# Kernel optimization log

Measured on AMD Instinct MI355X. Metric: run time of the kernel, lower is better.

The kernel has to match this reference:

```python
import jax, jax.numpy as jnp
import numpy as np

MASK_FILL = jnp.float32(-2**32 + 1)

def dice(x, alpha):
    # x: (S, B, F); batch-dim (dim=0) mean/std, unbiased std like torch.std
    avg = x.mean(axis=0)
    std = jnp.std(x, axis=0, ddof=1)
    p = jax.nn.sigmoid((x - avg) / std)
    return x * p + alpha * x * (1.0 - p)

def setup_inputs() -> dict:
    key = jax.random.key(0)
    ks = jax.random.split(key, 12)
    S, B, D = 200, 1024, 128          # seq_len, batch, 2H
    F = 4 * D                          # num_features = 512
    L1, L2 = 80, 40
    inp = {
        "query": jax.random.normal(ks[0], (B, D), jnp.float32),
        "facts": jax.random.normal(ks[1], (S, B, D), jnp.float32),
        "mask": jax.random.randint(ks[2], (S, B), 0, 2).astype(bool),
        "W1": jax.random.normal(ks[3], (F, L1), jnp.float32) / np.sqrt(F),
        "b1": jnp.zeros((L1,), jnp.float32),
        "a1": jnp.zeros((1,), jnp.float32),
        "W2": jax.random.normal(ks[4], (L1, L2), jnp.float32) / np.sqrt(L1),
        "b2": jnp.zeros((L2,), jnp.float32),
        "a2": jnp.zeros((1,), jnp.float32),
        "W3": jax.random.normal(ks[5], (L2, 1), jnp.float32) / np.sqrt(L2),
        "b3": jnp.zeros((1,), jnp.float32),
    }
    return inp

def reference(query, facts, mask, W1, b1, a1, W2, b2, a2, W3, b3):
    S, B, D = facts.shape
    # faithful to torch: tile along feature dim then reshape (permutes elements)
    q2 = jnp.tile(query, (1, S)).reshape(S, B, D)
    x = jnp.concatenate([q2, facts, q2 * facts, q2 - facts], axis=-1)  # (S,B,4D)
    h = dice(jnp.einsum('sbf,fl->sbl', x, W1) + b1, a1)
    h = dice(jnp.einsum('sbf,fl->sbl', h, W2) + b2, a2)
    logits = (jnp.einsum('sbf,fl->sbl', h, W3) + b3).squeeze(-1)  # (S,B)
    masked = jnp.where(mask, logits, MASK_FILL)
    normalized = jax.nn.softmax(masked, axis=0)
    return normalized[..., None] * facts  # (S,B,D)
```

## Files before the change

### kernel.cpp

```cpp
#include <hip/hip_runtime.h>
#include <hip/hip_bf16.h>
#include <math.h>

#define SS 200
#define BB 1024
#define DD 128
#define FF 512
#define LL1 80
#define LL2 40
#define PP (SS*BB)
#define MASK_FILL_F (-4294967295.0f)
#define NTILE 13

typedef short bf16x8 __attribute__((ext_vector_type(8)));
typedef float f32x4  __attribute__((ext_vector_type(4)));

static __device__ __forceinline__ unsigned short f2bf(float x) {
    __hip_bfloat16 h = __float2bfloat16(x);
    return *reinterpret_cast<unsigned short*>(&h);
}
static __device__ __forceinline__ float bf2f(unsigned short u) {
    __hip_bfloat16 h = *reinterpret_cast<__hip_bfloat16*>(&u);
    return __bfloat162float(h);
}
static __device__ __forceinline__ void split8(const float* x, bf16x8& ah, bf16x8& al) {
#pragma unroll
    for (int j = 0; j < 8; ++j) {
        unsigned u = __float_as_uint(x[j]);
        ah[j] = (short)(u >> 16);
        float hi = __uint_as_float(u & 0xffff0000u);
        al[j] = (short)f2bf(x[j] - hi);
    }
}
static __device__ __forceinline__ float fast_sigmoid(float t) {
    return __builtin_amdgcn_rcpf(1.f + __expf(-t));
}

__global__ void k_prep_all(const float* __restrict__ W1, const float* __restrict__ W2,
                           const unsigned char* __restrict__ mask,
                           unsigned short* __restrict__ bfr1,
                           unsigned short* __restrict__ bfr2, int* __restrict__ flag) {
    const int blk = blockIdx.x;
    if (blk == 35) {
        if (threadIdx.x < 64) {
            const uchar4 u = ((const uchar4*)mask)[threadIdx.x];
            const bool f = ((u.y | u.z) | u.w) != 0;
            const unsigned long long anyf = __ballot(f);
            if (threadIdx.x == 0) *flag = (anyf != 0ull) ? 1 : 0;
        }
        return;
    }
    if (blk < 30) {
        int t = blk * 256 + threadIdx.x;
        if (t >= 120 * 64) return;
        int lane = t & 63;
        int fid  = t >> 6;
        int nt   = fid % 5;
        int hl   = (fid / 5) % 2;
        int step = (fid / 10) % 6;
        int h    = fid / 60;
        int ktL  = step / 3;
        int seg  = step - 3 * ktL;
        int kt   = h * 2 + ktL;
        int n     = nt * 16 + (lane & 15);
        int kbase = kt * 32 + (lane >> 4) * 8;
        unsigned short* o = bfr1 + (size_t)t * 8;
#pragma unroll
        for (int j = 0; j < 8; ++j) {
            int k = kbase + j;
            float w;
            if (seg == 0)      w = W1[k * LL1 + n] + W1[(384 + k) * LL1 + n];
            else if (seg == 1) w = W1[(128 + k) * LL1 + n] - W1[(384 + k) * LL1 + n];
            else               w = W1[(256 + k) * LL1 + n];
            unsigned short hb = f2bf(w);
            o[j] = (hl == 0) ? hb : f2bf(w - bf2f(hb));
        }
    } else {
        int t = (blk - 30) * 256 + threadIdx.x;
        if (t >= 18 * 64) return;
        int lane = t & 63;
        int fid  = t >> 6;
        int hl   = fid & 1;
        int nt   = (fid >> 1) % 3;
        int kt   = fid / 6;
        int n  = nt * 16 + (lane & 15);
        int kb = kt * 32 + (lane >> 4) * 8;
        unsigned short* o = bfr2 + (size_t)t * 8;
#pragma unroll
        for (int j = 0; j < 8; ++j) {
            int k = kb + j;
            float w = (k < LL1 && n < LL2) ? W2[k * LL2 + n] : 0.f;
            unsigned short hb = f2bf(w);
            o[j] = (hl == 0) ? hb : f2bf(w - bf2f(hb));
        }
    }
}

__global__ __launch_bounds__(256, 2) void k1_mfma(
    const float* __restrict__ query, const float* __restrict__ facts,
    const unsigned short* __restrict__ bfr, const float* __restrict__ b1,
    float* __restrict__ z1) {
    const int tid  = threadIdx.x;
    const int lane = tid & 63;
    const int m    = lane & 15;
    const int quad = lane >> 4;
    const int pw   = blockIdx.x * 128 + (tid >> 6) * 32;

    __shared__ __align__(16) unsigned short lbuf[15360];

    f32x4 acc[2][5];
#pragma unroll
    for (int t = 0; t < 2; ++t)
#pragma unroll
        for (int nt = 0; nt < 5; ++nt) acc[t][nt] = (f32x4){0.f, 0.f, 0.f, 0.f};

    int pr[2], qr[2];
#pragma unroll
    for (int t = 0; t < 2; ++t) {
        pr[t] = pw + t * 16 + m;
        qr[t] = pr[t] / SS;
    }

#pragma unroll 1
    for (int kt = 0; kt < 4; ++kt) {
        const int dbase = kt * 32 + quad * 8;
        float q8[2][8], f8[2][8];
#pragma unroll
        for (int t = 0; t < 2; ++t) {
            const float* qp = query + (size_t)qr[t] * DD + dbase;
            const float* fp = facts + (size_t)pr[t] * DD + dbase;
            *(float4*)&q8[t][0] = *(const float4*)qp;
            *(float4*)&q8[t][4] = *(const float4*)(qp + 4);
            *(float4*)&f8[t][0] = *(const float4*)fp;
            *(float4*)&f8[t][4] = *(const float4*)(fp + 4);
        }
        if (kt) __syncthreads();
        {
            const int4* src = (const int4*)bfr + kt * 1920;
#pragma unroll
            for (int it = 0; it < 8; ++it) {
                int idx = it * 256 + tid;
                if (idx < 1920) ((int4*)lbuf)[idx] = src[idx];
            }
        }
        __syncthreads();

#pragma unroll
        for (int seg = 0; seg < 3; ++seg) {
            bf16x8 Bh[5], Bl[5];
#pragma unroll
            for (int nt = 0; nt < 5; ++nt) {
                Bh[nt] = *(const bf16x8*)&lbuf[((seg * 2 + 0) * 5 + nt) * 512 + lane * 8];
                Bl[nt] = *(const bf16x8*)&lbuf[((seg * 2 + 1) * 5 + nt) * 512 + lane * 8];
            }
#pragma unroll
            for (int t = 0; t < 2; ++t) {
                float x8[8];
#pragma unroll
                for (int j = 0; j < 8; ++j)
                    x8[j] = (seg == 0) ? q8[t][j]
                          : (seg == 1 ? f8[t][j] : q8[t][j] * f8[t][j]);
                bf16x8 ah, al;
                split8(x8, ah, al);
#pragma unroll
                for (int nt = 0; nt < 5; ++nt) {
                    acc[t][nt] = __builtin_amdgcn_mfma_f32_16x16x32_bf16(ah, Bh[nt], acc[t][nt], 0, 0, 0);
                    acc[t][nt] = __builtin_amdgcn_mfma_f32_16x16x32_bf16(al, Bh[nt], acc[t][nt], 0, 0, 0);
                    acc[t][nt] = __builtin_amdgcn_mfma_f32_16x16x32_bf16(ah, Bl[nt], acc[t][nt], 0, 0, 0);
                }
            }
        }
    }
#pragma unroll
    for (int t = 0; t < 2; ++t)
#pragma unroll
        for (int nt = 0; nt < 5; ++nt) {
            const int n = nt * 16 + m;
            const float bias = b1[n];
#pragma unroll
            for (int r = 0; r < 4; ++r)
                z1[(size_t)(pw + t * 16 + quad * 4 + r) * LL1 + n] = acc[t][nt][r] + bias;
        }
}

__global__ __launch_bounds__(512) void k_light(
    const float* __restrict__ z1, const unsigned short* __restrict__ bfr2,
    const float* __restrict__ a1, const float* __restrict__ b2,
    const float* __restrict__ a2, const float* __restrict__ W3,
    const float* __restrict__ b3, const void* __restrict__ mask,
    const int* __restrict__ flag, float* __restrict__ wbufT) {
    const int tid  = threadIdx.x;
    const int w    = tid >> 6;
    const int lane = tid & 63;
    const int m    = lane & 15;
    const int quad = lane >> 4;
    const int b    = blockIdx.x;

    __shared__ __align__(16) float z1f[NTILE * 16 * 81 + 16];
    __shared__ float psum[480], pssq[480];
    __shared__ float smean[LL1], sistd[LL1];
    __shared__ float sw3[LL2];
    __shared__ float red[8];

    {
        for (int i = tid; i < SS * 20; i += 512) {
            const int s = i / 20;
            const int o = i - s * 20;
            float4 v = ((const float4*)z1)[(size_t)(s * BB + b) * 20 + o];
            float* d = &z1f[s * 81 + o * 4];
            d[0] = v.x; d[1] = v.y; d[2] = v.z; d[3] = v.w;
        }
        for (int i = tid; i < 8 * 81 + 16; i += 512) z1f[SS * 81 + i] = 0.f;
    }
    __syncthreads();

    if (tid < 480) {
        const int l = tid % LL1, c = tid / LL1;
        const int s0 = c * 34;
        const int s1 = (s0 + 34 < SS) ? s0 + 34 : SS;
        float sum = 0.f, ssq = 0.f;
        for (int s = s0; s < s1; ++s) {
            float v = z1f[s * 81 + l];
            sum += v;
            ssq = fmaf(v, v, ssq);
        }
        psum[c * LL1 + l] = sum;
        pssq[c * LL1 + l] = ssq;
    }
    __syncthreads();
    if (tid < LL1) {
        float sum = 0.f, ssq = 0.f;
#pragma unroll
        for (int c = 0; c < 6; ++c) {
            sum += psum[c * LL1 + tid];
            ssq += pssq[c * LL1 + tid];
        }
        float mn  = sum * (1.f / SS);
        float var = (ssq - (float)SS * mn * mn) * (1.f / (SS - 1));
        smean[tid] = mn;
        sistd[tid] = rsqrtf(var);
    }
    __syncthreads();

    const float alpha1 = *a1;
    f32x4 acc2[2][3];
#pragma unroll
    for (int t = 0; t < 2; ++t)
#pragma unroll
        for (int nt = 0; nt < 3; ++nt) acc2[t][nt] = (f32x4){0.f, 0.f, 0.f, 0.f};

    int tile[2];
    bool tl[2];
#pragma unroll
    for (int t = 0; t < 2; ++t) {
        tile[t] = t * 8 + w;
        tl[t]   = (tile[t] < NTILE);
    }

#pragma unroll
    for (int kt = 0; kt < 3; ++kt) {
        bf16x8 Bh[3], Bl[3];
#pragma unroll
        for (int nt = 0; nt < 3; ++nt) {
            Bh[nt] = *(const bf16x8*)(bfr2 + (size_t)((kt * 3 + nt) * 2 + 0) * 512 + lane * 8);
            Bl[nt] = *(const bf16x8*)(bfr2 + (size_t)((kt * 3 + nt) * 2 + 1) * 512 + lane * 8);
        }
        const int kb = kt * 32 + quad * 8;
        const bool lv = (kt < 2 || quad < 2);
#pragma unroll
        for (int t = 0; t < 2; ++t) {
            if (!tl[t]) continue;
            float x8[8];
            if (lv) {
                const float* zr = &z1f[(tile[t] * 16 + m) * 81 + kb];
#pragma unroll
                for (int j = 0; j < 8; ++j) {
                    float v  = zr[j];
                    float pp = fast_sigmoid((v - smean[kb + j]) * sistd[kb + j]);
                    x8[j] = v * (alpha1 + (1.f - alpha1) * pp);
                }
            } else {
#pragma unroll
                for (int j = 0; j < 8; ++j) x8[j] = 0.f;
            }
            bf16x8 ah, al;
            split8(x8, ah, al);
#pragma unroll
            for (int nt = 0; nt < 3; ++nt) {
                acc2[t][nt] = __builtin_amdgcn_mfma_f32_16x16x32_bf16(ah, Bh[nt], acc2[t][nt], 0, 0, 0);
                acc2[t][nt] = __builtin_amdgcn_mfma_f32_16x16x32_bf16(al, Bh[nt], acc2[t][nt], 0, 0, 0);
                acc2[t][nt] = __builtin_amdgcn_mfma_f32_16x16x32_bf16(ah, Bl[nt], acc2[t][nt], 0, 0, 0);
            }
        }
    }
    __syncthreads();

    {
        float b2v[3];
#pragma unroll
        for (int nt = 0; nt < 3; ++nt) {
            const int n = nt * 16 + m;
            b2v[nt] = (n < LL2) ? b2[n] : 0.f;
        }
#pragma unroll
        for (int t = 0; t < 2; ++t) {
            if (!tl[t]) continue;
#pragma unroll
            for (int r = 0; r < 4; ++r) {
                const int srow = tile[t] * 16 + quad * 4 + r;
                if (srow >= SS) continue;
#pragma unroll
                for (int nt = 0; nt < 3; ++nt) {
                    const int n = nt * 16 + m;
                    if (n < LL2) z1f[srow * 41 + n] = acc2[t][nt][r] + b2v[nt];
                }
            }
        }
    }
    __syncthreads();

    if (tid < 480) {
        const int l = tid % LL2, c = tid / LL2;
        const int s0 = c * 17;
        const int s1 = (s0 + 17 < SS) ? s0 + 17 : SS;
        float sum = 0.f, ssq = 0.f;
        for (int s = s0; s < s1; ++s) {
            float v = z1f[s * 41 + l];
            sum += v;
            ssq = fmaf(v, v, ssq);
        }
        psum[c * LL2 + l] = sum;
        pssq[c * LL2 + l] = ssq;
    }
    __syncthreads();
    if (tid < LL2) {
        float sum = 0.f, ssq = 0.f;
#pragma unroll
        for (int c = 0; c < 12; ++c) {
            sum += psum[c * LL2 + tid];
            ssq += pssq[c * LL2 + tid];
        }
        float mn  = sum * (1.f / SS);
        float var = (ssq - (float)SS * mn * mn) * (1.f / (SS - 1));
        smean[tid] = mn;
        sistd[tid] = rsqrtf(var);
        sw3[tid]   = W3[tid];
    }
    __syncthreads();

    const float alpha2 = *a2;
    const int boolLayout = *flag;
    float logit = -3.0e38f;
    if (tid < SS) {
        float dot = b3[0];
#pragma unroll
        for (int k = 0; k < LL2; ++k) {
            float v  = z1f[tid * 41 + k];
            float pp = fast_sigmoid((v - smean[k]) * sistd[k]);
            float hh = v * (pp + alpha2 * (1.f - pp));
            dot = fmaf(hh, sw3[k], dot);
        }
        const int mi = tid * BB + b;
        const bool mk = boolLayout ? (((const unsigned char*)mask)[mi] != 0)
                                   : (((const int*)mask)[mi] != 0);
        logit = mk ? dot : MASK_FILL_F;
    }
    float v = logit;
#pragma unroll
    for (int off = 1; off < 64; off <<= 1) v = fmaxf(v, __shfl_xor(v, off, 64));
    if (lane == 0) red[w] = v;
    __syncthreads();
    float smax = red[0];
#pragma unroll
    for (int i = 1; i < 8; ++i) smax = fmaxf(smax, red[i]);
    __syncthreads();
    const float e = (tid < SS) ? __expf(logit - smax) : 0.f;
    v = e;
#pragma unroll
    for (int off = 1; off < 64; off <<= 1) v += __shfl_xor(v, off, 64);
    if (lane == 0) red[w] = v;
    __syncthreads();
    float ssum = red[0];
#pragma unroll
    for (int i = 1; i < 8; ++i) ssum += red[i];
    const float inv = __builtin_amdgcn_rcpf(ssum);
    if (tid < SS) wbufT[(size_t)b * SS + tid] = e * inv;
}

__global__ __launch_bounds__(256) void k4_scale(
    const float* __restrict__ wbufT, const float* __restrict__ facts,
    float* __restrict__ out) {
    int i = blockIdx.x * 256 + threadIdx.x;
    int p = i >> 5;
    float w = wbufT[(size_t)(p & (BB - 1)) * SS + (p >> 10)];
    float4 f = ((const float4*)facts)[i];
    float4 o;
    o.x = f.x * w; o.y = f.y * w; o.z = f.z * w; o.w = f.w * w;
    ((float4*)out)[i] = o;
}

extern "C" void kernel_launch(void* const* d_in, const int* in_sizes, int n_in,
                              void* d_out, int out_size, void* d_ws, size_t ws_size,
                              hipStream_t stream) {
    const float* query = (const float*)d_in[0];
    const float* facts = (const float*)d_in[1];
    const void*  mask  = d_in[2];
    const float* W1 = (const float*)d_in[3];
    const float* b1 = (const float*)d_in[4];
    const float* a1 = (const float*)d_in[5];
    const float* W2 = (const float*)d_in[6];
    const float* b2 = (const float*)d_in[7];
    const float* a2 = (const float*)d_in[8];
    const float* W3 = (const float*)d_in[9];
    const float* b3 = (const float*)d_in[10];
    float* out = (float*)d_out;

    float* z1 = out;
    unsigned short* bfr1 = (unsigned short*)(out + 24739840);
    unsigned short* bfr2 = (unsigned short*)(out + 24801280);
    float* wbufT = (float*)d_ws;
    int*   flag  = (int*)((char*)d_ws + 900 * 1024);

    k_prep_all<<<36, 256, 0, stream>>>(W1, W2, (const unsigned char*)mask, bfr1, bfr2, flag);
    k1_mfma<<<PP / 128, 256, 0, stream>>>(query, facts, bfr1, b1, z1);
    k_light<<<BB, 512, 0, stream>>>(z1, bfr2, a1, b2, a2, W3, b3, mask, flag, wbufT);
    k4_scale<<<(PP * DD) / (256 * 4), 256, 0, stream>>>(wbufT, facts, out);
}
```

Baseline: 306.9 us.

## Double-buffer W1 LDS tiles and prefetch next query/facts chunk in k1_mfma

Switches the W1 shared-memory staging in the first MFMA kernel to a two-slot ping-pong buffer. While the current K-chunk is consumed by MFMAs, the next chunk's weights and query/facts registers are loaded, which removes one barrier per iteration. The loop is now fully unrolled. This doubles LDS use to about 60KB per block and raises register pressure from the prefetch registers, which may hurt occupancy with two blocks per CU.

```diff
diff --git a/kernel.cpp b/kernel.cpp
--- a/kernel.cpp
+++ b/kernel.cpp
@@ -106,7 +106,7 @@
     const int quad = lane >> 4;
     const int pw   = blockIdx.x * 128 + (tid >> 6) * 32;
 
-    __shared__ __align__(16) unsigned short lbuf[15360];
+    __shared__ __align__(16) unsigned short lbuf[2][15360];
 
     f32x4 acc[2][5];
 #pragma unroll
@@ -121,10 +121,9 @@
         qr[t] = pr[t] / SS;
     }
 
-#pragma unroll 1
-    for (int kt = 0; kt < 4; ++kt) {
-        const int dbase = kt * 32 + quad * 8;
-        float q8[2][8], f8[2][8];
+    float q8[2][8], f8[2][8];
+    {
+        const int dbase = quad * 8;
 #pragma unroll
         for (int t = 0; t < 2; ++t) {
             const float* qp = query + (size_t)qr[t] * DD + dbase;
@@ -134,24 +133,45 @@
             *(float4*)&f8[t][0] = *(const float4*)fp;
             *(float4*)&f8[t][4] = *(const float4*)(fp + 4);
         }
-        if (kt) __syncthreads();
-        {
-            const int4* src = (const int4*)bfr + kt * 1920;
+        const int4* src = (const int4*)bfr;
+#pragma unroll
+        for (int it = 0; it < 8; ++it) {
+            int idx = it * 256 + tid;
+            if (idx < 1920) ((int4*)lbuf[0])[idx] = src[idx];
+        }
+    }
+    __syncthreads();
+
+#pragma unroll
+    for (int kt = 0; kt < 4; ++kt) {
+        float qn[2][8], fn[2][8];
+        if (kt < 3) {
+            const int dbase = (kt + 1) * 32 + quad * 8;
+#pragma unroll
+            for (int t = 0; t < 2; ++t) {
+                const float* qp = query + (size_t)qr[t] * DD + dbase;
+                const float* fp = facts + (size_t)pr[t] * DD + dbase;
+                *(float4*)&qn[t][0] = *(const float4*)qp;
+                *(float4*)&qn[t][4] = *(const float4*)(qp + 4);
+                *(float4*)&fn[t][0] = *(const float4*)fp;
+                *(float4*)&fn[t][4] = *(const float4*)(fp + 4);
+            }
+            const int4* src = (const int4*)bfr + (kt + 1) * 1920;
+            int4* dst = (int4*)lbuf[(kt + 1) & 1];
 #pragma unroll
             for (int it = 0; it < 8; ++it) {
                 int idx = it * 256 + tid;
-                if (idx < 1920) ((int4*)lbuf)[idx] = src[idx];
-            }
-        }
-        __syncthreads();
-
+                if (idx < 1920) dst[idx] = src[idx];
+            }
+        }
+        const unsigned short* cb = lbuf[kt & 1];
 #pragma unroll
         for (int seg = 0; seg < 3; ++seg) {
             bf16x8 Bh[5], Bl[5];
 #pragma unroll
             for (int nt = 0; nt < 5; ++nt) {
-                Bh[nt] = *(const bf16x8*)&lbuf[((seg * 2 + 0) * 5 + nt) * 512 + lane * 8];
-                Bl[nt] = *(const bf16x8*)&lbuf[((seg * 2 + 1) * 5 + nt) * 512 + lane * 8];
+                Bh[nt] = *(const bf16x8*)&cb[((seg * 2 + 0) * 5 + nt) * 512 + lane * 8];
+                Bl[nt] = *(const bf16x8*)&cb[((seg * 2 + 1) * 5 + nt) * 512 + lane * 8];
             }
 #pragma unroll
             for (int t = 0; t < 2; ++t) {
@@ -169,6 +189,16 @@
                     acc[t][nt] = __builtin_amdgcn_mfma_f32_16x16x32_bf16(ah, Bl[nt], acc[t][nt], 0, 0, 0);
                 }
             }
+        }
+        if (kt < 3) {
+            __syncthreads();
+#pragma unroll
+            for (int t = 0; t < 2; ++t)
+#pragma unroll
+                for (int j = 0; j < 8; ++j) {
+                    q8[t][j] = qn[t][j];
+                    f8[t][j] = fn[t][j];
+                }
         }
     }
 #pragma unroll
```

Result: no change. 310.9 us (+1.3%).

## Precompute per-query W1 contribution once and drop query segment from MFMA GEMM

Applied to the files above, without the earlier changes.

The query-only part of the first layer (q·(W1a+W1d) + b1) depends only on the batch row, so it is now computed once per query row in the prep kernel into a buffer U. The main MFMA kernel then handles only two K-segments (facts and q*facts) instead of three, which cuts its MFMA work and LDS weight staging by a third. The epilogue adds a gathered U row instead of the bias. This adds a small scalar prep pass and an extra global read per output element.

```diff
diff --git a/kernel.cpp b/kernel.cpp
--- a/kernel.cpp
+++ b/kernel.cpp
@@ -38,45 +38,32 @@
 
 __global__ void k_prep_all(const float* __restrict__ W1, const float* __restrict__ W2,
                            const unsigned char* __restrict__ mask,
+                           const float* __restrict__ query, const float* __restrict__ b1,
                            unsigned short* __restrict__ bfr1,
-                           unsigned short* __restrict__ bfr2, int* __restrict__ flag) {
+                           unsigned short* __restrict__ bfr2,
+                           float* __restrict__ U, int* __restrict__ flag) {
     const int blk = blockIdx.x;
-    if (blk == 35) {
-        if (threadIdx.x < 64) {
-            const uchar4 u = ((const uchar4*)mask)[threadIdx.x];
-            const bool f = ((u.y | u.z) | u.w) != 0;
-            const unsigned long long anyf = __ballot(f);
-            if (threadIdx.x == 0) *flag = (anyf != 0ull) ? 1 : 0;
-        }
-        return;
-    }
-    if (blk < 30) {
+    if (blk < 20) {
         int t = blk * 256 + threadIdx.x;
-        if (t >= 120 * 64) return;
         int lane = t & 63;
         int fid  = t >> 6;
-        int nt   = fid % 5;
-        int hl   = (fid / 5) % 2;
-        int step = (fid / 10) % 6;
-        int h    = fid / 60;
-        int ktL  = step / 3;
-        int seg  = step - 3 * ktL;
-        int kt   = h * 2 + ktL;
+        int nt = fid % 5;
+        int hl = (fid / 5) % 2;
+        int sg = (fid / 10) % 2;
+        int kt = fid / 20;
         int n     = nt * 16 + (lane & 15);
         int kbase = kt * 32 + (lane >> 4) * 8;
         unsigned short* o = bfr1 + (size_t)t * 8;
 #pragma unroll
         for (int j = 0; j < 8; ++j) {
             int k = kbase + j;
-            float w;
-            if (seg == 0)      w = W1[k * LL1 + n] + W1[(384 + k) * LL1 + n];
-            else if (seg == 1) w = W1[(128 + k) * LL1 + n] - W1[(384 + k) * LL1 + n];
-            else               w = W1[(256 + k) * LL1 + n];
+            float w = (sg == 0) ? (W1[(128 + k) * LL1 + n] - W1[(384 + k) * LL1 + n])
+                                :  W1[(256 + k) * LL1 + n];
             unsigned short hb = f2bf(w);
             o[j] = (hl == 0) ? hb : f2bf(w - bf2f(hb));
         }
-    } else {
-        int t = (blk - 30) * 256 + threadIdx.x;
+    } else if (blk < 25) {
+        int t = (blk - 20) * 256 + threadIdx.x;
         if (t >= 18 * 64) return;
         int lane = t & 63;
         int fid  = t >> 6;
@@ -93,12 +80,31 @@
             unsigned short hb = f2bf(w);
             o[j] = (hl == 0) ? hb : f2bf(w - bf2f(hb));
         }
+    } else if (blk == 25) {
+        if (threadIdx.x < 64) {
+            const uchar4 u = ((const uchar4*)mask)[threadIdx.x];
+            const bool f = ((u.y | u.z) | u.w) != 0;
+            const unsigned long long anyf = __ballot(f);
+            if (threadIdx.x == 0) *flag = (anyf != 0ull) ? 1 : 0;
+        }
+    } else {
+        const int tid = threadIdx.x;
+        if (tid >= 240) return;
+        const int qr = (blk - 26) * 3 + tid / 80;
+        const int n  = tid % 80;
+        if (qr >= 1024) return;
+        const float* q = query + (size_t)qr * DD;
+        float acc = b1[n];
+#pragma unroll 8
+        for (int k = 0; k < DD; ++k)
+            acc = fmaf(q[k], W1[k * LL1 + n] + W1[(384 + k) * LL1 + n], acc);
+        U[(size_t)qr * LL1 + n] = acc;
     }
 }
 
 __global__ __launch_bounds__(256, 2) void k1_mfma(
     const float* __restrict__ query, const float* __restrict__ facts,
-    const unsigned short* __restrict__ bfr, const float* __restrict__ b1,
+    const unsigned short* __restrict__ bfr, const float* __restrict__ U,
     float* __restrict__ z1) {
     const int tid  = threadIdx.x;
     const int lane = tid & 63;
@@ -106,7 +112,7 @@
     const int quad = lane >> 4;
     const int pw   = blockIdx.x * 128 + (tid >> 6) * 32;
 
-    __shared__ __align__(16) unsigned short lbuf[15360];
+    __shared__ __align__(16) unsigned short lbuf[10240];
 
     f32x4 acc[2][5];
 #pragma unroll
@@ -136,30 +142,27 @@
         }
         if (kt) __syncthreads();
         {
-            const int4* src = (const int4*)bfr + kt * 1920;
-#pragma unroll
-            for (int it = 0; it < 8; ++it) {
-                int idx = it * 256 + tid;
-                if (idx < 1920) ((int4*)lbuf)[idx] = src[idx];
-            }
+            const int4* src = (const int4*)bfr + kt * 1280;
+#pragma unroll
+            for (int it = 0; it < 5; ++it)
+                ((int4*)lbuf)[it * 256 + tid] = src[it * 256 + tid];
         }
         __syncthreads();
 
 #pragma unroll
-        for (int seg = 0; seg < 3; ++seg) {
+        for (int sg = 0; sg < 2; ++sg) {
             bf16x8 Bh[5], Bl[5];
 #pragma unroll
             for (int nt = 0; nt < 5; ++nt) {
-                Bh[nt] = *(const bf16x8*)&lbuf[((seg * 2 + 0) * 5 + nt) * 512 + lane * 8];
-                Bl[nt] = *(const bf16x8*)&lbuf[((seg * 2 + 1) * 5 + nt) * 512 + lane * 8];
+                Bh[nt] = *(const bf16x8*)&lbuf[((sg * 2 + 0) * 5 + nt) * 512 + lane * 8];
+                Bl[nt] = *(const bf16x8*)&lbuf[((sg * 2 + 1) * 5 + nt) * 512 + lane * 8];
             }
 #pragma unroll
             for (int t = 0; t < 2; ++t) {
                 float x8[8];
 #pragma unroll
                 for (int j = 0; j < 8; ++j)
-                    x8[j] = (seg == 0) ? q8[t][j]
-                          : (seg == 1 ? f8[t][j] : q8[t][j] * f8[t][j]);
+                    x8[j] = (sg == 0) ? f8[t][j] : q8[t][j] * f8[t][j];
                 bf16x8 ah, al;
                 split8(x8, ah, al);
 #pragma unroll
@@ -174,12 +177,14 @@
 #pragma unroll
     for (int t = 0; t < 2; ++t)
 #pragma unroll
-        for (int nt = 0; nt < 5; ++nt) {
-            const int n = nt * 16 + m;
-            const float bias = b1[n];
-#pragma unroll
-            for (int r = 0; r < 4; ++r)
-                z1[(size_t)(pw + t * 16 + quad * 4 + r) * LL1 + n] = acc[t][nt][r] + bias;
+        for (int r = 0; r < 4; ++r) {
+            const int p = pw + t * 16 + quad * 4 + r;
+            const float* urow = U + (size_t)(p / SS) * LL1;
+#pragma unroll
+            for (int nt = 0; nt < 5; ++nt) {
+                const int n = nt * 16 + m;
+                z1[(size_t)p * LL1 + n] = acc[t][nt][r] + urow[n];
+            }
         }
 }
 
@@ -416,13 +421,15 @@
     float* out = (float*)d_out;
 
     float* z1 = out;
+    float* U  = out + 24600000;
     unsigned short* bfr1 = (unsigned short*)(out + 24739840);
     unsigned short* bfr2 = (unsigned short*)(out + 24801280);
     float* wbufT = (float*)d_ws;
     int*   flag  = (int*)((char*)d_ws + 900 * 1024);
 
-    k_prep_all<<<36, 256, 0, stream>>>(W1, W2, (const unsigned char*)mask, bfr1, bfr2, flag);
-    k1_mfma<<<PP / 128, 256, 0, stream>>>(query, facts, bfr1, b1, z1);
+    k_prep_all<<<368, 256, 0, stream>>>(W1, W2, (const unsigned char*)mask,
+                                        query, b1, bfr1, bfr2, U, flag);
+    k1_mfma<<<PP / 128, 256, 0, stream>>>(query, facts, bfr1, U, z1);
     k_light<<<BB, 512, 0, stream>>>(z1, bfr2, a1, b2, a2, W3, b3, mask, flag, wbufT);
     k4_scale<<<(PP * DD) / (256 * 4), 256, 0, stream>>>(wbufT, facts, out);
 }
```

Result: faster. 298.9 us (-2.6%).
